# Kernel tuning notes

Hardware: AMD Instinct MI355X
Metric: run time of the kernel (lower is better)

## Reference

```python
import jax, jax.numpy as jnp
import numpy as np

B, C, N, K = 8, 3, 4096, 20
EPS = 1e-5

def bn(x, g, b, axes):
    # training-mode batch norm: normalize over batch/spatial axes, channel last
    m = jnp.mean(x, axes, keepdims=True)
    v = jnp.var(x, axes, keepdims=True)
    return g * (x - m) * jax.lax.rsqrt(v + EPS) + b

def setup_inputs() -> dict:
    key = jax.random.key(0)
    ks = jax.random.split(key, 8)
    def xav(kk, shape):
        fan_out, fan_in = shape
        lim = (6.0 / (fan_in + fan_out)) ** 0.5
        return jax.random.uniform(kk, shape, minval=-lim, maxval=lim, dtype=jnp.float32)
    return dict(
        x=jax.random.normal(ks[0], (B, C, N), dtype=jnp.float32),
        w1=xav(ks[1], (64, 2 * C)), g1=jnp.ones(64), b1=jnp.zeros(64),
        w2=xav(ks[2], (128, 64)), g2=jnp.ones(128), b2=jnp.zeros(128),
        w3=xav(ks[3], (1024, 128)), g3=jnp.ones(1024), b3=jnp.zeros(1024),
        w4=xav(ks[4], (512, 1024)), g4=jnp.ones(512), b4=jnp.zeros(512),
        w5=xav(ks[5], (256, 512)), g5=jnp.ones(256), b5=jnp.zeros(256),
        wl=jnp.zeros((9, 256), dtype=jnp.float32),  # zero-init per reset_parameters
        bl=jnp.zeros(9, dtype=jnp.float32),
    )

def reference(x, w1, g1, b1, w2, g2, b2, w3, g3, b3, w4, g4, b4, w5, g5, b5, wl, bl):
    xt = jnp.transpose(x, (0, 2, 1))  # (B, N, C)
    sq = jnp.sum(xt * xt, -1)  # (B, N)
    # negative squared pairwise distance: -(|a|^2 - 2ab + |b|^2)
    nd = 2.0 * jnp.einsum('bnc,bmc->bnm', xt, xt) - sq[:, :, None] - sq[:, None, :]
    _, idx = jax.lax.top_k(nd, K)  # (B, N, K) nearest neighbors (includes self)
    nbr = jax.vmap(lambda pts, ids: pts[ids])(xt, idx)  # (B, N, K, C)
    ctr = xt[:, :, None, :]
    edge = jnp.concatenate([jnp.broadcast_to(ctr, (B, N, K, C)), nbr - ctr], -1)  # (B,N,K,2C)
    # EdgeConv shared MLP (1x1 conv + BN + ReLU), then max over k
    h = jax.nn.relu(bn(jnp.einsum('bnkc,oc->bnko', edge, w1), g1, b1, (0, 1, 2)))
    h = jax.nn.relu(bn(jnp.einsum('bnkc,oc->bnko', h, w2), g2, b2, (0, 1, 2)))
    h = jnp.max(h, 2)  # (B, N, 128)
    # local shared MLP then global max pool over points
    h = jax.nn.relu(bn(jnp.einsum('bnc,oc->bno', h, w3), g3, b3, (0, 1)))
    h = jnp.max(h, 1)  # (B, 1024)
    # global MLP
    h = jax.nn.relu(bn(h @ w4.T, g4, b4, (0,)))
    h = jax.nn.relu(bn(h @ w5.T, g5, b5, (0,)))
    y = (h @ wl.T + bl).reshape(B, 3, 3)
    return y + jnp.eye(3, dtype=y.dtype)
```

## Files before the change

kernel.cpp:

```cpp
#include <hip/hip_runtime.h>

#define NPTS 4096
#define KNN 20
#define CNT1f 655360.0f
#define CNT3f 32768.0f
#define BNEPS 1e-5f

#define OFF_IDX   0
#define OFF_M     655360
#define OFF_ES    655360
#define OFF_G1P   656384
#define OFF_S1P   672768
#define ZERO1_BEG 655360
#define ZERO1_CNT 17664
#define OFF_W2B   2752512
#define OFF_W3B   2756608
#define OFF_XP    2822144
#define OFF_G3P   2953216
#define OFF_SM3P  2985984
#define OFF_GMAX  2986240
#define OFF_Z4    2994432
#define ZG3_BEG   2953216
#define ZG3_CNT   41216
#define OFF_SC1   4849664
#define OFF_SH1   4849728
#define OFF_SC2   4849792
#define OFF_SH2   4849920
#define OFF_SC3   4850048
#define OFF_SH3   4851072

typedef float f32x4 __attribute__((ext_vector_type(4)));
typedef short s16x8 __attribute__((ext_vector_type(8)));

__device__ __forceinline__ unsigned short f2bf(float f) {
    unsigned u = __float_as_uint(f);
    return (unsigned short)((u + 0x7FFFu + ((u >> 16) & 1u)) >> 16);
}

__global__ __launch_bounds__(256) void k_initprep(const float* __restrict__ x,
                                                  const float* __restrict__ w2,
                                                  const float* __restrict__ w3, float* W) {
    int i = blockIdx.x * 256 + threadIdx.x;
    unsigned short* w2b = (unsigned short*)(W + OFF_W2B);
    unsigned short* w3b = (unsigned short*)(W + OFF_W3B);
    w3b[i] = f2bf(w3[i]);
    if (i < 8192) w2b[i] = f2bf(w2[i]);
    if (i < ZERO1_CNT) W[ZERO1_BEG + i] = 0.0f;
    if (i < ZG3_CNT) W[ZG3_BEG + i] = 0.0f;
    if (i < 32768) {
        int b = i >> 12, j = i & 4095;
        float4 p;
        p.x = x[b * 12288 + j];
        p.y = x[b * 12288 + 4096 + j];
        p.z = x[b * 12288 + 8192 + j];
        p.w = 0.f;
        ((float4*)(W + OFF_XP))[i] = p;
    }
}

template <int PER>
__device__ __forceinline__ void wave_scan_find(const int* H, int K, int lane,
                                               int& B, int& below, int& hB) {
    int c[PER]; int s = 0;
    const int base = lane * PER;
#pragma unroll
    for (int p = 0; p < PER; ++p) { c[p] = H[base + p]; s += c[p]; }
    int pre = s;
#pragma unroll
    for (int off = 1; off < 64; off <<= 1) {
        int t = __shfl_up(pre, off, 64);
        if (lane >= off) pre += t;
    }
    int excl = pre - s;
    bool has = (excl < K) && (K <= excl + s);
    unsigned long long m = __ballot(has);
    int src = (int)(__ffsll((unsigned long long)m) - 1);
    int mb = 0, mbelow = 0, mh = 0;
    if (lane == src) {
        int cum = excl;
#pragma unroll
        for (int p = 0; p < PER; ++p) {
            if (cum < K && K <= cum + c[p]) { mb = base + p; mbelow = cum; mh = c[p]; break; }
            cum += c[p];
        }
    }
    B = __shfl(mb, src, 64);
    below = __shfl(mbelow, src, 64);
    hB = __shfl(mh, src, 64);
}

__global__ __launch_bounds__(256) void k_knn(int* __restrict__ idx, float* W) {
    __shared__ int hist[2][512];
    __shared__ int outi[2][20];
    __shared__ int cnts[2][2];
    __shared__ unsigned int minsh[2][2];
    __shared__ float estat[27];
    const int tid = threadIdx.x;
    const int b = blockIdx.y;
    const float4* xb4 = ((const float4*)(W + OFF_XP)) + b * NPTS;
    if (tid < 27) estat[tid] = 0.f;
    if (tid < 4) cnts[tid >> 1][tid & 1] = 0;
    const int wv = tid >> 6, lane = tid & 63;
    const int pair = wv >> 1, half = wv & 1;
    const int tid128 = tid & 127;
    const int q = blockIdx.x * 2 + pair;
    const float4 qp = xb4[q];
    int* H = hist[pair];
#pragma unroll
    for (int p = 0; p < 4; ++p) H[tid128 * 4 + p] = 0;
    unsigned int key[32];
    unsigned int mymin = 0xFFFFFFFFu;
#pragma unroll
    for (int it = 0; it < 32; ++it) {
        int j = it * 128 + tid128;
        float4 pp = xb4[j];
        float dx = pp.x - qp.x, dy = pp.y - qp.y, dz = pp.z - qp.z;
        float d = fmaf(dx, dx, fmaf(dy, dy, dz * dz));
        unsigned int u = (j == q) ? 0xFFFFFFFFu : __float_as_uint(d);
        key[it] = u;
        mymin = mymin < u ? mymin : u;
    }
#pragma unroll
    for (int off = 32; off; off >>= 1) {
        unsigned int o = (unsigned int)__shfl_xor((int)mymin, off);
        mymin = mymin < o ? mymin : o;
    }
    if (lane == 0) minsh[pair][half] = mymin;
    __syncthreads();
    const unsigned int base = minsh[pair][0] < minsh[pair][1] ? minsh[pair][0] : minsh[pair][1];
#pragma unroll
    for (int it = 0; it < 32; ++it) {
        unsigned int t9 = key[it] - base;
        unsigned int bin = t9 >> 20; if (bin > 511u) bin = 511u;
        atomicAdd(&H[bin], 1);
    }
    __syncthreads();
    int B, below, hB;
    wave_scan_find<8>(H, KNN - 1, lane, B, below, hB);
    unsigned int P = (unsigned int)B;
    int rem = (KNN - 1) - below;
    int S = 20;
    bool fin = (hB == rem);
    __syncthreads();
    if (!fin) {
#pragma unroll
        for (int p = 0; p < 4; ++p) H[tid128 * 4 + p] = 0;
    }
    __syncthreads();
    if (!fin) {
#pragma unroll
        for (int it = 0; it < 32; ++it) {
            unsigned int t9 = key[it] - base;
            unsigned int b0 = t9 >> 20; if (b0 > 511u) b0 = 511u;
            if (b0 == P) atomicAdd(&H[(t9 >> 11) & 511], 1);
        }
    }
    __syncthreads();
    if (!fin) {
        wave_scan_find<8>(H, rem, lane, B, below, hB);
        P = (P << 9) | (unsigned int)B;
        rem -= below;
        S = 11;
        fin = (hB == rem);
    }
    __syncthreads();
    if (!fin) {
#pragma unroll
        for (int p = 0; p < 4; ++p) H[tid128 * 4 + p] = 0;
    }
    __syncthreads();
    if (!fin) {
#pragma unroll
        for (int it = 0; it < 32; ++it) {
            unsigned int t9 = key[it] - base;
            if ((t9 >> 11) == P) atomicAdd(&H[(t9 >> 2) & 511], 1);
        }
    }
    __syncthreads();
    if (!fin) {
        wave_scan_find<8>(H, rem, lane, B, below, hB);
        P = (P << 9) | (unsigned int)B;
        rem -= below;
        S = 2;
    }
    int* OC = cnts[pair];
#pragma unroll
    for (int it = 0; it < 32; ++it) {
        unsigned int t9 = key[it] - base;
        unsigned int v;
        if (S == 20) { v = t9 >> 20; if (v > 511u) v = 511u; }
        else v = t9 >> S;
        if (v <= P) {
            bool take = v < P;
            if (!take) { int e = atomicAdd(&OC[1], 1); take = (e < rem); }
            if (take) { int pos = atomicAdd(&OC[0], 1); outi[pair][pos] = it * 128 + tid128; }
        }
    }
    if (half == 0 && lane == 0) outi[pair][KNN - 1] = q;
    __syncthreads();
    const int obase = (b * NPTS + q) * KNN;
    if (half == 0 && lane < KNN) idx[obase + lane] = outi[pair][lane];
    float st[27];
#pragma unroll
    for (int v = 0; v < 27; ++v) st[v] = 0.f;
    if (half == 0 && lane < KNN) {
        int j = outi[pair][lane];
        float4 np = xb4[j];
        float e[6];
        e[0] = qp.x; e[1] = qp.y; e[2] = qp.z;
        e[3] = np.x - qp.x; e[4] = np.y - qp.y; e[5] = np.z - qp.z;
        int id = 6;
#pragma unroll
        for (int i = 0; i < 6; ++i) {
            st[i] = e[i];
#pragma unroll
            for (int jj = i; jj < 6; ++jj) { st[id] = e[i] * e[jj]; id++; }
        }
    }
    if (half == 0) {
#pragma unroll
        for (int v = 0; v < 27; ++v) {
            float s = st[v];
            s += __shfl_xor(s, 32); s += __shfl_xor(s, 16); s += __shfl_xor(s, 8);
            s += __shfl_xor(s, 4);  s += __shfl_xor(s, 2);  s += __shfl_xor(s, 1);
            st[v] = s;
        }
        if (lane == 0) {
#pragma unroll
            for (int v = 0; v < 27; ++v) atomicAdd(&estat[v], st[v]);
        }
    }
    __syncthreads();
    if (tid < 27) atomicAdd(&W[OFF_ES + (blockIdx.x & 31) * 32 + tid], estat[tid]);
}

__global__ void k_fin1(const float* __restrict__ w1, const float* __restrict__ g1,
                       const float* __restrict__ b1, float* W) {
    __shared__ float es[27];
    const int c = threadIdx.x;
    if (c < 27) {
        float s = 0.f;
        for (int p = 0; p < 32; ++p) s += W[OFF_ES + p * 32 + c];
        es[c] = s;
    }
    __syncthreads();
    float wr[6];
#pragma unroll
    for (int i = 0; i < 6; ++i) wr[i] = w1[c * 6 + i];
    float m = 0.f;
#pragma unroll
    for (int i = 0; i < 6; ++i) m += wr[i] * es[i];
    m *= (1.f / CNT1f);
    float qv = 0.f;
    int id = 6;
#pragma unroll
    for (int i = 0; i < 6; ++i)
#pragma unroll
        for (int jj = 0; jj < 6; ++jj)
            if (jj >= i) { qv += (jj == i ? 1.f : 2.f) * wr[i] * wr[jj] * es[id]; id++; }
    qv *= (1.f / CNT1f);
    float var = qv - m * m;
    float sc = g1[c] * rsqrtf(var + BNEPS);
    W[OFF_SC1 + c] = sc;
    W[OFF_SH1 + c] = b1[c] - m * sc;
}

__global__ __launch_bounds__(256) void k_gram1(const int* __restrict__ idx,
                                               const float* __restrict__ w1, float* W) {
    __shared__ unsigned short h1t[80 * 136];
    __shared__ float eds[128 * 6];
    __shared__ float w1s[64 * 6];
    __shared__ float sc1s[64], sh1s[64];
    const int t = threadIdx.x;
    const int b = blockIdx.x >> 6;
    const int ebase_b = (blockIdx.x & 63) * 1280;
    const float4* xpb = ((const float4*)(W + OFF_XP)) + b * NPTS;
    if (t < 384) w1s[t] = w1[t];
    if (t < 64) { sc1s[t] = W[OFF_SC1 + t]; sh1s[t] = W[OFF_SH1 + t]; }
    for (int i = t; i < 2048; i += 256) {
        int rr = i >> 7, e = i & 127;
        h1t[(64 + rr) * 136 + e] = (rr == 0) ? (unsigned short)0x3F80 : (unsigned short)0;
    }
    const int w = t >> 6, lane = t & 63, n16 = lane & 15, quad = lane >> 4;
    f32x4 acc[5];
#pragma unroll
    for (int j = 0; j < 5; ++j) acc[j] = (f32x4){0.f, 0.f, 0.f, 0.f};
    for (int ck = 0; ck < 10; ++ck) {
        __syncthreads();
        if (t < 128) {
            int e_l = ebase_b + ck * 128 + t;
            int q = e_l / KNN;
            int jn = idx[b * (NPTS * KNN) + e_l];
            float4 c = xpb[q];
            float4 n = xpb[jn];
            float* E = &eds[t * 6];
            E[0] = c.x; E[1] = c.y; E[2] = c.z;
            E[3] = n.x - c.x; E[4] = n.y - c.y; E[5] = n.z - c.z;
        }
        __syncthreads();
        {
            const int e128 = t & 127, half = t >> 7;
            float e0 = eds[e128 * 6 + 0], e1 = eds[e128 * 6 + 1], e2 = eds[e128 * 6 + 2];
            float e3 = eds[e128 * 6 + 3], e4 = eds[e128 * 6 + 4], e5 = eds[e128 * 6 + 5];
#pragma unroll 4
            for (int cc = 0; cc < 32; ++cc) {
                int c = half * 32 + cc;
                const float* wr = &w1s[c * 6];
                float z = wr[0] * e0 + wr[1] * e1 + wr[2] * e2 + wr[3] * e3 + wr[4] * e4 + wr[5] * e5;
                float h = sc1s[c] * z + sh1s[c];
                h1t[c * 136 + e128] = f2bf(h > 0.f ? h : 0.f);
            }
        }
        __syncthreads();
#pragma unroll
        for (int ks = 0; ks < 4; ++ks) {
            s16x8 Af = *(const s16x8*)&h1t[(w * 16 + n16) * 136 + ks * 32 + quad * 8];
#pragma unroll
            for (int jt = 0; jt < 5; ++jt) {
                s16x8 Bf = *(const s16x8*)&h1t[(jt * 16 + n16) * 136 + ks * 32 + quad * 8];
                acc[jt] = __builtin_amdgcn_mfma_f32_16x16x32_bf16(Af, Bf, acc[jt], 0, 0, 0);
            }
        }
    }
    const int part = blockIdx.x & 3;
    const int gi = w * 16 + quad * 4;
#pragma unroll
    for (int jt = 0; jt < 4; ++jt)
#pragma unroll
        for (int r = 0; r < 4; ++r)
            atomicAdd(&W[OFF_G1P + part * 4096 + (gi + r) * 64 + jt * 16 + n16], acc[jt][r]);
    if (n16 == 0) {
#pragma unroll
        for (int r = 0; r < 4; ++r)
            atomicAdd(&W[OFF_S1P + part * 64 + gi + r], acc[4][r]);
    }
}

__global__ __launch_bounds__(256) void k_fin2(const float* __restrict__ w2, const float* __restrict__ g2,
                                              const float* __restrict__ b2, float* W) {
    __shared__ float Gs[4096];
    __shared__ float s1s[64];
    __shared__ float w2s[128 * 65];
    const int t = threadIdx.x;
    for (int i = t; i < 4096; i += 256)
        Gs[i] = W[OFF_G1P + i] + W[OFF_G1P + 4096 + i] + W[OFF_G1P + 8192 + i] + W[OFF_G1P + 12288 + i];
    if (t < 64) s1s[t] = W[OFF_S1P + t] + W[OFF_S1P + 64 + t] + W[OFF_S1P + 128 + t] + W[OFF_S1P + 192 + t];
    for (int i = t; i < 8192; i += 256) w2s[(i >> 6) * 65 + (i & 63)] = w2[i];
    __syncthreads();
    const int c = t >> 1, half = t & 1;
    float acc = 0.f;
    for (int ii = 0; ii < 32; ++ii) {
        int i = 32 * half + ii;
        float wi = w2s[c * 65 + i];
        float inner = 0.f;
        for (int j = 0; j < 64; ++j) inner += Gs[i * 64 + j] * w2s[c * 65 + j];
        acc += wi * inner;
    }
    acc += __shfl_xor(acc, 1);
    if (half == 0) {
        float ms = 0.f;
        for (int j = 0; j < 64; ++j) ms += w2s[c * 65 + j] * s1s[j];
        float mean = ms * (1.f / CNT1f);
        float var = acc * (1.f / CNT1f) - mean * mean;
        float sc = g2[c] * rsqrtf(var + BNEPS);
        W[OFF_SC2 + c] = sc;
        W[OFF_SH2 + c] = b2[c] - mean * sc;
    }
}

__global__ __launch_bounds__(256) void k_c2apply(const int* __restrict__ idx,
                                                 const float* __restrict__ w1, float* W) {
    __shared__ unsigned short h1b[256 * 72];
    __shared__ float eds[160 * 6];
    const int t = threadIdx.x;
    const int b = blockIdx.y, q0 = blockIdx.x * 8;
    const float4* xpb = ((const float4*)(W + OFF_XP)) + b * NPTS;
    const int ebase = (b * NPTS + q0) * KNN;
    const unsigned short* w2b = (const unsigned short*)(W + OFF_W2B);
    if (t < 160) {
        int q = q0 + t / KNN;
        int jn = idx[ebase + t];
        float4 c = xpb[q];
        float4 n = xpb[jn];
        float* E = &eds[t * 6];
        E[0] = c.x; E[1] = c.y; E[2] = c.z;
        E[3] = n.x - c.x; E[4] = n.y - c.y; E[5] = n.z - c.z;
    }
    __syncthreads();
    {
        const int j64 = t & 63, grp = t >> 6;
        float wr[6];
#pragma unroll
        for (int i = 0; i < 6; ++i) wr[i] = w1[j64 * 6 + i];
        const float sc = W[OFF_SC1 + j64], sh = W[OFF_SH1 + j64];
        for (int qq = grp * 2; qq < grp * 2 + 2; ++qq) {
#pragma unroll 4
            for (int kk = 0; kk < 32; ++kk) {
                float v = 0.f;
                if (kk < 20) {
                    const float* E = &eds[(qq * 20 + kk) * 6];
                    float z = wr[0] * E[0] + wr[1] * E[1] + wr[2] * E[2] + wr[3] * E[3] + wr[4] * E[4] + wr[5] * E[5];
                    float h = sc * z + sh;
                    v = h > 0.f ? h : 0.f;
                }
                h1b[(qq * 32 + kk) * 72 + j64] = f2bf(v);
            }
        }
    }
    __syncthreads();
    const int w = t >> 6, lane = t & 63, n16 = lane & 15, quad = lane >> 4;
    unsigned short* Mb = (unsigned short*)(W + OFF_M);
#pragma unroll
    for (int nt_i = 0; nt_i < 2; ++nt_i) {
        const int nt = 2 * w + nt_i;
        const int chan = nt * 16 + n16;
        const float sc2 = W[OFF_SC2 + chan], sh2 = W[OFF_SH2 + chan];
        s16x8 Bf0 = *(const s16x8*)&w2b[chan * 64 + quad * 8];
        s16x8 Bf1 = *(const s16x8*)&w2b[chan * 64 + 32 + quad * 8];
#pragma unroll
        for (int q = 0; q < 8; ++q) {
            f32x4 accA = (f32x4){0.f, 0.f, 0.f, 0.f};
            f32x4 accB = (f32x4){0.f, 0.f, 0.f, 0.f};
            s16x8 a0 = *(const s16x8*)&h1b[(q * 32 + n16) * 72 + quad * 8];
            s16x8 a1 = *(const s16x8*)&h1b[(q * 32 + 16 + n16) * 72 + quad * 8];
            accA = __builtin_amdgcn_mfma_f32_16x16x32_bf16(a0, Bf0, accA, 0, 0, 0);
            accB = __builtin_amdgcn_mfma_f32_16x16x32_bf16(a1, Bf0, accB, 0, 0, 0);
            a0 = *(const s16x8*)&h1b[(q * 32 + n16) * 72 + 32 + quad * 8];
            a1 = *(const s16x8*)&h1b[(q * 32 + 16 + n16) * 72 + 32 + quad * 8];
            accA = __builtin_amdgcn_mfma_f32_16x16x32_bf16(a0, Bf1, accA, 0, 0, 0);
            accB = __builtin_amdgcn_mfma_f32_16x16x32_bf16(a1, Bf1, accB, 0, 0, 0);
            float mx = 0.f;
#pragma unroll
            for (int r = 0; r < 4; ++r) {
                float h = sc2 * accA[r] + sh2;
                mx = fmaxf(mx, h > 0.f ? h : 0.f);
            }
            if (quad == 0) {
#pragma unroll
                for (int r = 0; r < 4; ++r) {
                    float h = sc2 * accB[r] + sh2;
                    mx = fmaxf(mx, h > 0.f ? h : 0.f);
                }
            }
            mx = fmaxf(mx, __shfl_xor(mx, 16));
            mx = fmaxf(mx, __shfl_xor(mx, 32));
            if (quad == 0)
                Mb[(b * NPTS + q0 + q) * 128 + chan] = f2bf(mx);
        }
    }
}

__global__ __launch_bounds__(256) void k_gram3(float* W) {
    __shared__ unsigned short Mt[128 * 72];
    const int t = threadIdx.x;
    const int w = t >> 6, lane = t & 63, n16 = lane & 15, quad = lane >> 4;
    const int r0 = blockIdx.x * 512;
    const unsigned int* Msrc = (const unsigned int*)(W + OFF_M);
    const int nA = 8 - w;
    f32x4 acc[9];
#pragma unroll
    for (int j = 0; j < 9; ++j) acc[j] = (f32x4){0.f, 0.f, 0.f, 0.f};
    float smacc = 0.f;
    for (int ch = 0; ch < 8; ++ch) {
        __syncthreads();
        for (int i = t; i < 4096; i += 256) {
            int row = i >> 6, c2 = i & 63;
            unsigned int v = Msrc[(r0 + ch * 64 + row) * 64 + c2];
            Mt[(2 * c2) * 72 + row]     = (unsigned short)(v & 0xFFFFu);
            Mt[(2 * c2 + 1) * 72 + row] = (unsigned short)(v >> 16);
        }
        __syncthreads();
#pragma unroll
        for (int j = 0; j < 9; ++j) {
            int ti = (j < nA) ? w : (7 - w);
            int tj = (j < nA) ? (w + j) : (j - nA + 7 - w);
#pragma unroll
            for (int ks = 0; ks < 2; ++ks) {
                s16x8 Af = *(const s16x8*)&Mt[(ti * 16 + n16) * 72 + ks * 32 + quad * 8];
                s16x8 Bf = *(const s16x8*)&Mt[(tj * 16 + n16) * 72 + ks * 32 + quad * 8];
                acc[j] = __builtin_amdgcn_mfma_f32_16x16x32_bf16(Af, Bf, acc[j], 0, 0, 0);
            }
        }
        if (t < 128) {
            float s = 0.f;
            for (int e = 0; e < 64; ++e)
                s += __uint_as_float((unsigned int)Mt[t * 72 + e] << 16);
            smacc += s;
        }
    }
    const int part = blockIdx.x & 1;
    float* Gp = &W[OFF_G3P + part * 16384];
#pragma unroll
    for (int j = 0; j < 9; ++j) {
        int ti = (j < nA) ? w : (7 - w);
        int tj = (j < nA) ? (w + j) : (j - nA + 7 - w);
#pragma unroll
        for (int r = 0; r < 4; ++r)
            atomicAdd(&Gp[(ti * 16 + quad * 4 + r) * 128 + tj * 16 + n16], acc[j][r]);
    }
    if (t < 128) atomicAdd(&W[OFF_SM3P + part * 128 + t], smacc);
}

__global__ __launch_bounds__(256) void k_fin3(const float* __restrict__ w3, const float* __restrict__ g3,
                                              const float* __restrict__ b3, float* W) {
    __shared__ float G3s[128 * 129];
    __shared__ float w3s[16 * 132];
    __shared__ float sm3[128];
    __shared__ float red[256];
    __shared__ float mred[16];
    const int t = threadIdx.x;
    const int c0 = blockIdx.x * 16;
    for (int i = t; i < 16384; i += 256) {
        int row = i >> 7, col = i & 127;
        int src = ((row >> 4) <= (col >> 4)) ? (row * 128 + col) : (col * 128 + row);
        G3s[row * 129 + col] = W[OFF_G3P + src] + W[OFF_G3P + 16384 + src];
    }
    for (int i = t; i < 2048; i += 256)
        w3s[(i >> 7) * 132 + (i & 127)] = w3[(c0 + (i >> 7)) * 128 + (i & 127)];
    if (t < 128) sm3[t] = W[OFF_SM3P + t] + W[OFF_SM3P + 128 + t];
    __syncthreads();
    const int cl = t >> 4, seg = t & 15;
    float acc = 0.f;
    for (int ii = 0; ii < 8; ++ii) {
        int i = 8 * seg + ii;
        float wi = w3s[cl * 132 + i];
        float inner = 0.f;
        for (int j = 0; j < 128; ++j) inner += G3s[i * 129 + j] * w3s[cl * 132 + j];
        acc += wi * inner;
    }
    red[t] = acc;
    if (seg == 0) {
        float ms = 0.f;
        for (int j = 0; j < 128; ++j) ms += w3s[cl * 132 + j] * sm3[j];
        mred[cl] = ms;
    }
    __syncthreads();
    if (t < 16) {
        float s = 0.f;
#pragma unroll
        for (int k = 0; k < 16; ++k) s += red[t * 16 + k];
        float mean = mred[t] * (1.f / CNT3f);
        float var = s * (1.f / CNT3f) - mean * mean;
        float sc = g3[c0 + t] * rsqrtf(var + BNEPS);
        W[OFF_SC3 + c0 + t] = sc;
        W[OFF_SH3 + c0 + t] = b3[c0 + t] - mean * sc;
    }
}

__global__ __launch_bounds__(256) void k_conv3(float* W) {
    __shared__ unsigned short Mt[64 * 136];
    const int t = threadIdx.x;
    const int p0 = blockIdx.x * 64, c0g = blockIdx.y * 128;
    const unsigned int* Msrc = (const unsigned int*)(W + OFF_M);
    const unsigned short* w3b = (const unsigned short*)(W + OFF_W3B);
    for (int i = t; i < 4096; i += 256) {
        int row = i >> 6, c2 = i & 63;
        *(unsigned int*)&Mt[row * 136 + 2 * c2] = Msrc[(p0 + row) * 64 + c2];
    }
    __syncthreads();
    const int w = t >> 6, lane = t & 63, n16 = lane & 15, quad = lane >> 4;
    const int bbatch = p0 >> 12;
#pragma unroll
    for (int nt_i = 0; nt_i < 2; ++nt_i) {
        const int nt = 2 * w + nt_i;
        const int chan = c0g + nt * 16 + n16;
        const float sc3 = W[OFF_SC3 + chan], sh3 = W[OFF_SH3 + chan];
        s16x8 Bf[4];
#pragma unroll
        for (int ks = 0; ks < 4; ++ks)
            Bf[ks] = *(const s16x8*)&w3b[chan * 128 + ks * 32 + quad * 8];
        float mx = 0.f;
#pragma unroll
        for (int mt = 0; mt < 4; ++mt) {
            f32x4 acc = (f32x4){0.f, 0.f, 0.f, 0.f};
#pragma unroll
            for (int ks = 0; ks < 4; ++ks) {
                s16x8 Af = *(const s16x8*)&Mt[(mt * 16 + n16) * 136 + ks * 32 + quad * 8];
                acc = __builtin_amdgcn_mfma_f32_16x16x32_bf16(Af, Bf[ks], acc, 0, 0, 0);
            }
#pragma unroll
            for (int r = 0; r < 4; ++r) {
                float h = sc3 * acc[r] + sh3;
                mx = fmaxf(mx, h > 0.f ? h : 0.f);
            }
        }
        mx = fmaxf(mx, __shfl_xor(mx, 16));
        mx = fmaxf(mx, __shfl_xor(mx, 32));
        if (quad == 0)
            atomicMax((unsigned int*)&W[OFF_GMAX + bbatch * 1024 + chan], __float_as_uint(mx));
    }
}

__global__ __launch_bounds__(256) void k_fc4(const float* __restrict__ w4, float* W) {
    __shared__ float red[256];
    const int t = threadIdx.x;
    const int oidx = t >> 3, s = t & 7;
    const int cc = oidx >> 3, b = oidx & 7;
    const int c = blockIdx.x * 4 + cc;
    const float* g = &W[OFF_GMAX];
    const float* wr = &w4[c * 1024 + s * 128];
    const float* gr = &g[b * 1024 + s * 128];
    float p = 0.f;
    for (int j = 0; j < 128; ++j) p += wr[j] * gr[j];
    red[t] = p;
    __syncthreads();
    if (t < 32) {
        float tot = 0.f;
        for (int k = 0; k < 8; ++k) tot += red[t * 8 + k];
        W[OFF_Z4 + (t & 7) * 512 + blockIdx.x * 4 + (t >> 3)] = tot;
    }
}

__global__ __launch_bounds__(512) void k_tail(const float* __restrict__ g4, const float* __restrict__ b4,
                                              const float* __restrict__ w5, const float* __restrict__ g5,
                                              const float* __restrict__ b5, const float* __restrict__ wl,
                                              const float* __restrict__ bl, float* W, float* __restrict__ out) {
    __shared__ float h4L[8 * 512];
    __shared__ float w5s[2 * 256 * 9];
    __shared__ float zp[2 * 2048];
    const int t = threadIdx.x;
    {
        float v[8]; float s = 0.f, q = 0.f;
#pragma unroll
        for (int b = 0; b < 8; ++b) { v[b] = W[OFF_Z4 + b * 512 + t]; s += v[b]; q += v[b] * v[b]; }
        float mean = s * 0.125f;
        float var = q * 0.125f - mean * mean;
        float sc = g4[t] * rsqrtf(var + BNEPS);
        float sh = b4[t] - mean * sc;
#pragma unroll
        for (int b = 0; b < 8; ++b) {
            float h = sc * v[b] + sh;
            h4L[b * 512 + t] = h > 0.f ? h : 0.f;
        }
    }
    const int c5 = t & 255, half = t >> 8;
    float acc[8];
#pragma unroll
    for (int b = 0; b < 8; ++b) acc[b] = 0.f;
    for (int jt = 0; jt < 32; ++jt) {
        __syncthreads();
        for (int i = t; i < 4096; i += 512) {
            int h = i >> 11, rem = i & 2047;
            int ci = rem >> 3, jj = rem & 7;
            w5s[h * 2304 + ci * 9 + jj] = w5[ci * 512 + h * 256 + jt * 8 + jj];
        }
        __syncthreads();
#pragma unroll
        for (int jj = 0; jj < 8; ++jj) {
            float wv = w5s[half * 2304 + c5 * 9 + jj];
            int jg = half * 256 + jt * 8 + jj;
#pragma unroll
            for (int b = 0; b < 8; ++b) acc[b] += wv * h4L[b * 512 + jg];
        }
    }
#pragma unroll
    for (int b = 0; b < 8; ++b) zp[half * 2048 + b * 256 + c5] = acc[b];
    __syncthreads();
    if (t < 256) {
        float v[8], s = 0.f, q = 0.f;
#pragma unroll
        for (int b = 0; b < 8; ++b) {
            v[b] = zp[b * 256 + t] + zp[2048 + b * 256 + t];
            s += v[b]; q += v[b] * v[b];
        }
        float mean = s * 0.125f, var = q * 0.125f - mean * mean;
        float sc = g5[t] * rsqrtf(var + BNEPS), sh = b5[t] - mean * sc;
#pragma unroll
        for (int b = 0; b < 8; ++b) { float h = sc * v[b] + sh; zp[b * 256 + t] = h > 0.f ? h : 0.f; }
    }
    __syncthreads();
    if (t < 72) {
        int b = t / 9, r = t % 9;
        float a = bl[r] + ((r == 0 || r == 4 || r == 8) ? 1.f : 0.f);
        for (int j = 0; j < 256; ++j) a += wl[r * 256 + j] * zp[b * 256 + j];
        out[b * 9 + r] = a;
    }
}

extern "C" void kernel_launch(void* const* d_in, const int* in_sizes, int n_in,
                              void* d_out, int out_size, void* d_ws, size_t ws_size,
                              hipStream_t stream) {
    const float* x  = (const float*)d_in[0];
    const float* w1 = (const float*)d_in[1];
    const float* g1 = (const float*)d_in[2];
    const float* b1 = (const float*)d_in[3];
    const float* w2 = (const float*)d_in[4];
    const float* g2 = (const float*)d_in[5];
    const float* b2 = (const float*)d_in[6];
    const float* w3 = (const float*)d_in[7];
    const float* g3 = (const float*)d_in[8];
    const float* b3 = (const float*)d_in[9];
    const float* w4 = (const float*)d_in[10];
    const float* g4 = (const float*)d_in[11];
    const float* b4 = (const float*)d_in[12];
    const float* w5 = (const float*)d_in[13];
    const float* g5 = (const float*)d_in[14];
    const float* b5 = (const float*)d_in[15];
    const float* wl = (const float*)d_in[16];
    const float* bl = (const float*)d_in[17];
    float* W = (float*)d_ws;
    int* idx = (int*)d_ws;
    float* out = (float*)d_out;

    k_initprep<<<dim3(512), dim3(256), 0, stream>>>(x, w2, w3, W);
    k_knn<<<dim3(2048, 8), dim3(256), 0, stream>>>(idx, W);
    k_fin1<<<dim3(1), dim3(64), 0, stream>>>(w1, g1, b1, W);
    k_gram1<<<dim3(512), dim3(256), 0, stream>>>(idx, w1, W);
    k_fin2<<<dim3(1), dim3(256), 0, stream>>>(w2, g2, b2, W);
    k_c2apply<<<dim3(512, 8), dim3(256), 0, stream>>>(idx, w1, W);
    k_gram3<<<dim3(64), dim3(256), 0, stream>>>(W);
    k_fin3<<<dim3(64), dim3(256), 0, stream>>>(w3, g3, b3, W);
    k_conv3<<<dim3(512, 8), dim3(256), 0, stream>>>(W);
    k_fc4<<<dim3(128), dim3(256), 0, stream>>>(w4, W);
    k_tail<<<dim3(1), dim3(512), 0, stream>>>(g4, b4, w5, g5, b5, wl, bl, W, out);
}
```

Measured before the change: 607.6 us.

## Split single-block FC5 tail into parallel kernels and widen KNN first-pass histogram

The one-block tail kernel, which computed BN4, the 512-to-256 FC5 layer and the final head serially, is split into three kernels. The middle one, k_fc5, spreads the FC5 matrix-vector work across 64 blocks, removing a long serial single-block stage. Separately, the KNN radix-select first-pass histogram grows from 512 to 1024 bins (shift 19 instead of 20), which should make it less likely that the later refinement passes are needed. The trade-off is two extra kernel launches and a larger shared-memory histogram per block.

```diff
diff --git a/kernel.cpp b/kernel.cpp
--- a/kernel.cpp
+++ b/kernel.cpp
@@ -28,6 +28,8 @@
 #define OFF_SH2   4849920
 #define OFF_SC3   4850048
 #define OFF_SH3   4851072
+#define OFF_H4    4852096
+#define OFF_Z5    4856192
 
 typedef float f32x4 __attribute__((ext_vector_type(4)));
 typedef short s16x8 __attribute__((ext_vector_type(8)));
@@ -90,7 +92,7 @@
 }
 
 __global__ __launch_bounds__(256) void k_knn(int* __restrict__ idx, float* W) {
-    __shared__ int hist[2][512];
+    __shared__ int hist[2][1024];
     __shared__ int outi[2][20];
     __shared__ int cnts[2][2];
     __shared__ unsigned int minsh[2][2];
@@ -107,7 +109,7 @@
     const float4 qp = xb4[q];
     int* H = hist[pair];
 #pragma unroll
-    for (int p = 0; p < 4; ++p) H[tid128 * 4 + p] = 0;
+    for (int p = 0; p < 8; ++p) H[tid128 * 8 + p] = 0;
     unsigned int key[32];
     unsigned int mymin = 0xFFFFFFFFu;
 #pragma unroll
@@ -131,15 +133,15 @@
 #pragma unroll
     for (int it = 0; it < 32; ++it) {
         unsigned int t9 = key[it] - base;
-        unsigned int bin = t9 >> 20; if (bin > 511u) bin = 511u;
+        unsigned int bin = t9 >> 19; if (bin > 1023u) bin = 1023u;
         atomicAdd(&H[bin], 1);
     }
     __syncthreads();
     int B, below, hB;
-    wave_scan_find<8>(H, KNN - 1, lane, B, below, hB);
+    wave_scan_find<16>(H, KNN - 1, lane, B, below, hB);
     unsigned int P = (unsigned int)B;
     int rem = (KNN - 1) - below;
-    int S = 20;
+    int S = 19;
     bool fin = (hB == rem);
     __syncthreads();
     if (!fin) {
@@ -151,8 +153,8 @@
 #pragma unroll
         for (int it = 0; it < 32; ++it) {
             unsigned int t9 = key[it] - base;
-            unsigned int b0 = t9 >> 20; if (b0 > 511u) b0 = 511u;
-            if (b0 == P) atomicAdd(&H[(t9 >> 11) & 511], 1);
+            unsigned int b0 = t9 >> 19; if (b0 > 1023u) b0 = 1023u;
+            if (b0 == P) atomicAdd(&H[(t9 >> 10) & 511], 1);
         }
     }
     __syncthreads();
@@ -160,7 +162,7 @@
         wave_scan_find<8>(H, rem, lane, B, below, hB);
         P = (P << 9) | (unsigned int)B;
         rem -= below;
-        S = 11;
+        S = 10;
         fin = (hB == rem);
     }
     __syncthreads();
@@ -173,7 +175,7 @@
 #pragma unroll
         for (int it = 0; it < 32; ++it) {
             unsigned int t9 = key[it] - base;
-            if ((t9 >> 11) == P) atomicAdd(&H[(t9 >> 2) & 511], 1);
+            if ((t9 >> 10) == P) atomicAdd(&H[(t9 >> 1) & 511], 1);
         }
     }
     __syncthreads();
@@ -181,14 +183,14 @@
         wave_scan_find<8>(H, rem, lane, B, below, hB);
         P = (P << 9) | (unsigned int)B;
         rem -= below;
-        S = 2;
+        S = 1;
     }
     int* OC = cnts[pair];
 #pragma unroll
     for (int it = 0; it < 32; ++it) {
         unsigned int t9 = key[it] - base;
         unsigned int v;
-        if (S == 20) { v = t9 >> 20; if (v > 511u) v = 511u; }
+        if (S == 19) { v = t9 >> 19; if (v > 1023u) v = 1023u; }
         else v = t9 >> S;
         if (v <= P) {
             bool take = v < P;
@@ -611,56 +613,52 @@
     }
 }
 
-__global__ __launch_bounds__(512) void k_tail(const float* __restrict__ g4, const float* __restrict__ b4,
-                                              const float* __restrict__ w5, const float* __restrict__ g5,
-                                              const float* __restrict__ b5, const float* __restrict__ wl,
-                                              const float* __restrict__ bl, float* W, float* __restrict__ out) {
-    __shared__ float h4L[8 * 512];
-    __shared__ float w5s[2 * 256 * 9];
-    __shared__ float zp[2 * 2048];
+__global__ __launch_bounds__(512) void k_fin4(const float* __restrict__ g4, const float* __restrict__ b4,
+                                              float* W) {
+    const int t = threadIdx.x;
+    float v[8]; float s = 0.f, q = 0.f;
+#pragma unroll
+    for (int b = 0; b < 8; ++b) { v[b] = W[OFF_Z4 + b * 512 + t]; s += v[b]; q += v[b] * v[b]; }
+    float mean = s * 0.125f;
+    float var = q * 0.125f - mean * mean;
+    float sc = g4[t] * rsqrtf(var + BNEPS);
+    float sh = b4[t] - mean * sc;
+#pragma unroll
+    for (int b = 0; b < 8; ++b) {
+        float h = sc * v[b] + sh;
+        W[OFF_H4 + b * 512 + t] = h > 0.f ? h : 0.f;
+    }
+}
+
+__global__ __launch_bounds__(256) void k_fc5(const float* __restrict__ w5, float* W) {
+    __shared__ float red[256];
+    const int t = threadIdx.x;
+    const int c4 = t >> 6, b = (t >> 3) & 7, s = t & 7;
+    const int c = blockIdx.x * 4 + c4;
+    const float* wr = &w5[c * 512 + s * 64];
+    const float* hr = &W[OFF_H4 + b * 512 + s * 64];
+    float p = 0.f;
+    for (int j = 0; j < 64; ++j) p += wr[j] * hr[j];
+    red[t] = p;
+    __syncthreads();
+    if (t < 32) {
+        const int cc = t >> 3, bb = t & 7;
+        float tot = 0.f;
+        for (int k = 0; k < 8; ++k) tot += red[cc * 64 + bb * 8 + k];
+        W[OFF_Z5 + bb * 256 + blockIdx.x * 4 + cc] = tot;
+    }
+}
+
+__global__ __launch_bounds__(256) void k_tail2(const float* __restrict__ g5, const float* __restrict__ b5,
+                                               const float* __restrict__ wl, const float* __restrict__ bl,
+                                               float* W, float* __restrict__ out) {
+    __shared__ float zp[2048];
     const int t = threadIdx.x;
     {
-        float v[8]; float s = 0.f, q = 0.f;
-#pragma unroll
-        for (int b = 0; b < 8; ++b) { v[b] = W[OFF_Z4 + b * 512 + t]; s += v[b]; q += v[b] * v[b]; }
-        float mean = s * 0.125f;
-        float var = q * 0.125f - mean * mean;
-        float sc = g4[t] * rsqrtf(var + BNEPS);
-        float sh = b4[t] - mean * sc;
+        float v[8], s = 0.f, q = 0.f;
 #pragma unroll
         for (int b = 0; b < 8; ++b) {
-            float h = sc * v[b] + sh;
-            h4L[b * 512 + t] = h > 0.f ? h : 0.f;
-        }
-    }
-    const int c5 = t & 255, half = t >> 8;
-    float acc[8];
-#pragma unroll
-    for (int b = 0; b < 8; ++b) acc[b] = 0.f;
-    for (int jt = 0; jt < 32; ++jt) {
-        __syncthreads();
-        for (int i = t; i < 4096; i += 512) {
-            int h = i >> 11, rem = i & 2047;
-            int ci = rem >> 3, jj = rem & 7;
-            w5s[h * 2304 + ci * 9 + jj] = w5[ci * 512 + h * 256 + jt * 8 + jj];
-        }
-        __syncthreads();
-#pragma unroll
-        for (int jj = 0; jj < 8; ++jj) {
-            float wv = w5s[half * 2304 + c5 * 9 + jj];
-            int jg = half * 256 + jt * 8 + jj;
-#pragma unroll
-            for (int b = 0; b < 8; ++b) acc[b] += wv * h4L[b * 512 + jg];
-        }
-    }
-#pragma unroll
-    for (int b = 0; b < 8; ++b) zp[half * 2048 + b * 256 + c5] = acc[b];
-    __syncthreads();
-    if (t < 256) {
-        float v[8], s = 0.f, q = 0.f;
-#pragma unroll
-        for (int b = 0; b < 8; ++b) {
-            v[b] = zp[b * 256 + t] + zp[2048 + b * 256 + t];
+            v[b] = W[OFF_Z5 + b * 256 + t];
             s += v[b]; q += v[b] * v[b];
         }
         float mean = s * 0.125f, var = q * 0.125f - mean * mean;
@@ -712,5 +710,7 @@
     k_fin3<<<dim3(64), dim3(256), 0, stream>>>(w3, g3, b3, W);
     k_conv3<<<dim3(512, 8), dim3(256), 0, stream>>>(W);
     k_fc4<<<dim3(128), dim3(256), 0, stream>>>(w4, W);
-    k_tail<<<dim3(1), dim3(512), 0, stream>>>(g4, b4, w5, g5, b5, wl, bl, W, out);
-}
+    k_fin4<<<dim3(1), dim3(512), 0, stream>>>(g4, b4, W);
+    k_fc5<<<dim3(64), dim3(256), 0, stream>>>(w5, W);
+    k_tail2<<<dim3(1), dim3(256), 0, stream>>>(g5, b5, wl, bl, W, out);
+}
```

Result: faster. 549.6 us (-9.5%).
